# Optimization experiments

Measured on AMD Instinct MI355X. Metric: run time of the kernel, lower is better.

The kernel has to match this reference:

```python
import jax, jax.numpy as jnp
import numpy as np
from jax import lax

T, B, C = 2048, 8, 1024
H, K, P = 16, 31, 15  # num_heads, kernel_size, padding_l
R = C // H


def setup_inputs() -> dict:
    key = jax.random.key(0)
    k1, k2 = jax.random.split(key)
    x = jax.random.normal(k1, (T, B, C), dtype=jnp.float32)
    # xavier_uniform for (H, 1, K): gain*sqrt(6/(fan_in+fan_out)) with fan_in=K, fan_out=1
    limit = float(np.sqrt(6.0 / (K + 1)))
    weight = jax.random.uniform(k2, (H, 1, K), dtype=jnp.float32, minval=-limit, maxval=limit)
    bias = jnp.zeros((C,), dtype=jnp.float32)
    return {"x": x, "weight": weight, "bias": bias}


def reference(x, weight, bias):
    # x: (T, B, C); weight: (H, 1, K); bias: (C,)
    w = jax.nn.softmax(weight.reshape(H, K), axis=1)       # weight_softmax=True
    w_ch = jnp.repeat(w, R, axis=0)                        # (C, K) per-channel depthwise filters
    x_nct = jnp.transpose(x, (1, 2, 0))                    # (B, C, T)
    # depthwise cross-correlation, 'same' padding: left P, right K-1-P
    out = lax.conv_general_dilated(
        x_nct, w_ch[:, None, :],                           # kernel (O=C, I/g=1, K)
        window_strides=(1,), padding=[(P, K - 1 - P)],
        feature_group_count=C,
        dimension_numbers=("NCH", "OIH", "NCH"),
    )                                                      # (B, C, T)
    return jnp.transpose(out, (2, 0, 1)) + bias            # (T, B, C)
```

## Files before the change

kernel.cpp:

```cpp
#include <hip/hip_runtime.h>
#include <math.h>


#define T_DIM 2048
#define B_DIM 8
#define C_DIM 1024
#define H_DIM 16
#define K_DIM 31
#define P_PAD 15
#define STRIP 16
#define WIN (STRIP + K_DIM - 1)

template<bool CHECK>
__device__ __forceinline__ void run_strip(const float* __restrict__ xb,
                                          float* __restrict__ ob,
                                          const float (&w)[K_DIM],
                                          float bv, int t0)
{
    float xr[WIN];
    #pragma unroll
    for (int r = 0; r < WIN; ++r) {
        const int t = t0 - P_PAD + r;
        float xv = 0.f;
        if (!CHECK || ((unsigned)t < (unsigned)T_DIM)) {
            xv = xb[(size_t)t * (B_DIM * C_DIM)];
        }
        xr[r] = xv;
    }
    __builtin_amdgcn_sched_barrier(0);

    float acc[STRIP];
    #pragma unroll
    for (int i = 0; i < STRIP; ++i) acc[i] = bv;

    #pragma unroll
    for (int r = 0; r < WIN; ++r) {
        const float xv = xr[r];
        #pragma unroll
        for (int i = 0; i < STRIP; ++i) {
            const int k = r - i;
            if (k >= 0 && k < K_DIM) {
                acc[i] = fmaf(xv, w[k], acc[i]);
            }
        }
    }

    #pragma unroll
    for (int i = 0; i < STRIP; ++i) {
        __builtin_nontemporal_store(acc[i], &ob[(size_t)(t0 + i) * (B_DIM * C_DIM)]);
    }
}

__global__ __launch_bounds__(256)
__attribute__((amdgpu_waves_per_eu(2, 4)))
void lwconv_tbc_kernel(
    const float* __restrict__ x,
    const float* __restrict__ weight,
    const float* __restrict__ bias,
    float* __restrict__ out)
{
    const int tid  = threadIdx.x;
    const int lane = tid & 63;
    const int c    = blockIdx.x * 256 + tid;
    const int h    = c >> 6;
    const int b    = blockIdx.y;
    const int t0   = blockIdx.z * STRIP;

    float wv = -1e30f;
    if (lane < K_DIM) wv = weight[h * K_DIM + lane];
    float m = wv;
    #pragma unroll
    for (int off = 32; off; off >>= 1) m = fmaxf(m, __shfl_xor(m, off));
    float e = (lane < K_DIM) ? expf(wv - m) : 0.f;
    float s = e;
    #pragma unroll
    for (int off = 32; off; off >>= 1) s += __shfl_xor(s, off);
    const float p = e / s;

    float w[K_DIM];
    #pragma unroll
    for (int k = 0; k < K_DIM; ++k) {
        union { float f; int i; } u;
        u.f = p;
        u.i = __builtin_amdgcn_readlane(u.i, k);
        w[k] = u.f;
    }

    const float bv = bias[c];
    const float* xb = x + (size_t)b * C_DIM + c;
    float* ob = out + (size_t)b * C_DIM + c;

    const bool interior = (t0 >= P_PAD) && (t0 + STRIP - 1 + K_DIM - 1 - P_PAD < T_DIM);
    if (interior) run_strip<false>(xb, ob, w, bv, t0);
    else          run_strip<true >(xb, ob, w, bv, t0);
}

extern "C" void kernel_launch(void* const* d_in, const int* in_sizes, int n_in,
                              void* d_out, int out_size, void* d_ws, size_t ws_size,
                              hipStream_t stream) {
    const float* x      = (const float*)d_in[0];
    const float* weight = (const float*)d_in[1];
    const float* bias   = (const float*)d_in[2];
    float* out = (float*)d_out;

    dim3 grid(C_DIM / 256, B_DIM, T_DIM / STRIP);
    dim3 block(256);
    lwconv_tbc_kernel<<<grid, block, 0, stream>>>(x, weight, bias, out);
}
```

Baseline: 29.14 us.

## Vectorize channels to float4 per thread and split wave into four time strips

Each thread now handles four consecutive channels with 128-bit loads and stores. Each wave covers one head, and its four 16-lane groups take adjacent 8-step time strips. The strip length is halved, the explicit register preload of the input window and the sched_barrier are removed, and the waves_per_eu hint is dropped. The aim is fewer, wider memory instructions and less shared per-thread overhead (softmax, readlane) per output element. In exchange the window overlap ratio per strip rises and register pressure grows from the four-wide accumulators.

```diff
diff --git a/kernel.cpp b/kernel.cpp
--- a/kernel.cpp
+++ b/kernel.cpp
@@ -8,51 +8,49 @@
 #define H_DIM 16
 #define K_DIM 31
 #define P_PAD 15
-#define STRIP 16
+#define STRIP 8
+#define GROUPS 4
+#define SUPER (STRIP * GROUPS)
 #define WIN (STRIP + K_DIM - 1)
 
+typedef float f32x4 __attribute__((ext_vector_type(4)));
+
 template<bool CHECK>
-__device__ __forceinline__ void run_strip(const float* __restrict__ xb,
-                                          float* __restrict__ ob,
-                                          const float (&w)[K_DIM],
-                                          float bv, int t0)
+__device__ __forceinline__ void run_strip4(const float* __restrict__ xb,
+                                           float* __restrict__ ob,
+                                           const float (&w)[K_DIM],
+                                           const f32x4 bv, int t0)
 {
-    float xr[WIN];
-    #pragma unroll
-    for (int r = 0; r < WIN; ++r) {
-        const int t = t0 - P_PAD + r;
-        float xv = 0.f;
-        if (!CHECK || ((unsigned)t < (unsigned)T_DIM)) {
-            xv = xb[(size_t)t * (B_DIM * C_DIM)];
-        }
-        xr[r] = xv;
-    }
-    __builtin_amdgcn_sched_barrier(0);
-
-    float acc[STRIP];
+    f32x4 acc[STRIP];
     #pragma unroll
     for (int i = 0; i < STRIP; ++i) acc[i] = bv;
 
     #pragma unroll
     for (int r = 0; r < WIN; ++r) {
-        const float xv = xr[r];
+        const int t = t0 - P_PAD + r;
+        f32x4 xv = (f32x4)(0.f);
+        if (!CHECK || ((unsigned)t < (unsigned)T_DIM)) {
+            xv = *reinterpret_cast<const f32x4*>(&xb[(size_t)t * (B_DIM * C_DIM)]);
+        }
         #pragma unroll
         for (int i = 0; i < STRIP; ++i) {
             const int k = r - i;
             if (k >= 0 && k < K_DIM) {
-                acc[i] = fmaf(xv, w[k], acc[i]);
+                #pragma unroll
+                for (int j = 0; j < 4; ++j)
+                    acc[i][j] = fmaf(xv[j], w[k], acc[i][j]);
             }
         }
     }
 
     #pragma unroll
     for (int i = 0; i < STRIP; ++i) {
-        __builtin_nontemporal_store(acc[i], &ob[(size_t)(t0 + i) * (B_DIM * C_DIM)]);
+        __builtin_nontemporal_store(
+            acc[i], reinterpret_cast<f32x4*>(&ob[(size_t)(t0 + i) * (B_DIM * C_DIM)]));
     }
 }
 
 __global__ __launch_bounds__(256)
-__attribute__((amdgpu_waves_per_eu(2, 4)))
 void lwconv_tbc_kernel(
     const float* __restrict__ x,
     const float* __restrict__ weight,
@@ -61,17 +59,21 @@
 {
     const int tid  = threadIdx.x;
     const int lane = tid & 63;
-    const int c    = blockIdx.x * 256 + tid;
-    const int h    = c >> 6;
-    const int b    = blockIdx.y;
-    const int t0   = blockIdx.z * STRIP;
+    const int wv_i = tid >> 6;
+    const int g    = lane >> 4;
+    const int l16  = lane & 15;
 
-    float wv = -1e30f;
-    if (lane < K_DIM) wv = weight[h * K_DIM + lane];
-    float m = wv;
+    const int h  = blockIdx.x * 4 + wv_i;
+    const int c  = h * 64 + l16 * 4;
+    const int b  = blockIdx.y;
+    const int t0 = blockIdx.z * SUPER + g * STRIP;
+
+    float wvv = -1e30f;
+    if (lane < K_DIM) wvv = weight[h * K_DIM + lane];
+    float m = wvv;
     #pragma unroll
     for (int off = 32; off; off >>= 1) m = fmaxf(m, __shfl_xor(m, off));
-    float e = (lane < K_DIM) ? expf(wv - m) : 0.f;
+    float e = (lane < K_DIM) ? expf(wvv - m) : 0.f;
     float s = e;
     #pragma unroll
     for (int off = 32; off; off >>= 1) s += __shfl_xor(s, off);
@@ -86,13 +88,15 @@
         w[k] = u.f;
     }
 
-    const float bv = bias[c];
+    const f32x4 bv = *reinterpret_cast<const f32x4*>(&bias[c]);
     const float* xb = x + (size_t)b * C_DIM + c;
     float* ob = out + (size_t)b * C_DIM + c;
 
-    const bool interior = (t0 >= P_PAD) && (t0 + STRIP - 1 + K_DIM - 1 - P_PAD < T_DIM);
-    if (interior) run_strip<false>(xb, ob, w, bv, t0);
-    else          run_strip<true >(xb, ob, w, bv, t0);
+    if (blockIdx.z == 0 || blockIdx.z == (T_DIM / SUPER) - 1) {
+        run_strip4<true >(xb, ob, w, bv, t0);
+    } else {
+        run_strip4<false>(xb, ob, w, bv, t0);
+    }
 }
 
 extern "C" void kernel_launch(void* const* d_in, const int* in_sizes, int n_in,
@@ -103,7 +107,7 @@
     const float* bias   = (const float*)d_in[2];
     float* out = (float*)d_out;
 
-    dim3 grid(C_DIM / 256, B_DIM, T_DIM / STRIP);
+    dim3 grid(H_DIM / 4, B_DIM, T_DIM / SUPER);
     dim3 block(256);
     lwconv_tbc_kernel<<<grid, block, 0, stream>>>(x, weight, bias, out);
 }
```

After: 30.71 us. +5.4%, slower.
